# Performance work log

Hardware: AMD Instinct MI355X
Metric: run time of the kernel (lower is better)

## Reference

```python
import jax, jax.numpy as jnp
import numpy as np

B, T, D_IN, H, D_OUT, L = 8, 4096, 256, 1024, 256, 2


def setup_inputs() -> dict:
    key = jax.random.key(0)
    ks = jax.random.split(key, 8)
    def w(k, shape, fan):
        return (jax.random.normal(k, shape, jnp.float32) / np.sqrt(fan)).astype(jnp.float32)
    return dict(
        x=jax.random.normal(ks[0], (B, T, D_IN), jnp.float32),
        start=jax.random.randint(ks[1], (B, T), 0, 2).astype(bool),
        Wi=w(ks[2], (H, D_IN), D_IN), bi=jnp.zeros((H,), jnp.float32),
        Wp=w(ks[3], (L, H, H), H), bp=jnp.zeros((L, H), jnp.float32),
        Wf=w(ks[4], (L, H, 2 * H), 2 * H), bf=jnp.zeros((L, H), jnp.float32),
        Wo=w(ks[5], (D_OUT, H), H), bo=jnp.zeros((D_OUT,), jnp.float32),
    )


def _reset_scan(z, flags, carry0):
    # Resettable(LogBayesMonoid) segmented additive scan.
    # z: [B,T,H] log-likelihood increments, flags: [B,T] start flags, carry0: [B,1,H].
    states = jnp.concatenate([carry0, z], axis=1)                      # [B,T+1,H]
    f = jnp.concatenate([jnp.zeros_like(flags[:, :1]), flags], axis=1)  # [B,T+1]
    def combine(a, b):
        sa, fa = a
        sb, fb = b
        # reset-aware monoid combine: if b starts an episode, drop a's state
        return (jnp.where(fb[..., None], sb, sa + sb), fa | fb)
    s_all, _ = jax.lax.associative_scan(combine, (states, f), axis=1)
    return s_all[:, 1:]                                                # [B,T,H]


def reference(x, start, Wi, bi, Wp, bp, Wf, bf, Wo, bo):
    emb = jnp.einsum('btd,hd->bth', x, Wi) + bi                         # map_in
    hdim = Wi.shape[0]
    carry0 = jnp.full((x.shape[0], 1, hdim), -jnp.log(jnp.float32(hdim)), x.dtype)
    layer_in = emb
    for l in range(Wp.shape[0]):
        z = jnp.einsum('bth,gh->btg', layer_in, Wp[l]) + bp[l]          # forward_map project
        states = _reset_scan(z, start, carry0)                          # log-Bayes accumulation
        out = jax.nn.softmax(states, axis=-1)                           # backward_map readout
        cat = jnp.concatenate([out, emb], axis=-1)                      # [B,T,2H]
        layer_in = jax.nn.leaky_relu(jnp.einsum('btc,hc->bth', cat, Wf[l]) + bf[l])
    return jnp.einsum('bth,oh->bto', layer_in, Wo) + bo                 # map_out
```

## Files before the change

### kernel.cpp

```cpp
#include <hip/hip_runtime.h>
#include <stdint.h>

typedef unsigned short ushort_t;
typedef __attribute__((ext_vector_type(4))) float f32x4;
typedef __attribute__((ext_vector_type(8))) short bf16x8;
typedef __attribute__((ext_vector_type(4))) unsigned short u16x4;

#define DEV static __device__ __forceinline__

DEV unsigned short f2bf(float f) {
  unsigned int u = __float_as_uint(f);
  unsigned int r = (u + 0x7fffu + ((u >> 16) & 1u)) >> 16;
  return (unsigned short)r;
}

DEV float bf2f(ushort_t u) { return __uint_as_float((unsigned)u << 16); }

DEV float4 ld_bf4(const ushort_t* p) {
  const u16x4 u = *(const u16x4*)p;
  float4 v;
  v.x = bf2f(u.x); v.y = bf2f(u.y); v.z = bf2f(u.z); v.w = bf2f(u.w);
  return v;
}

DEV void async16(const void* g, void* l) {
  __builtin_amdgcn_global_load_lds(
      (const __attribute__((address_space(1))) unsigned int*)g,
      (__attribute__((address_space(3))) unsigned int*)l, 16, 0, 0);
}

template<bool SPLIT, bool RELU, bool OUTBF16>
__global__ __launch_bounds__(256, 2)
void gemm_bt(const ushort_t* __restrict__ A0, int lda0,
             const ushort_t* __restrict__ A1, int lda1,
             const ushort_t* __restrict__ W0, int ldw0,
             const ushort_t* __restrict__ W1, int ldw1,
             int K0, int K,
             const float* __restrict__ bias,
             void* __restrict__ Cv, int ldc,
             int rowsPerBatch, int cBatchStrideRows, int cRowOff)
{
  __shared__ __align__(16) ushort_t sA[2][128 * 32];
  __shared__ __align__(16) ushort_t sB[2][128 * 32];

  const int tid = threadIdx.x;
  const int w = tid >> 6, lane = tid & 63;

  const int NTl = gridDim.x;
  const int wgid = blockIdx.y * NTl + blockIdx.x;
  const int X = wgid & 7, j = wgid >> 3;
  const int n_t = j % NTl, mg = j / NTl;
  const int mBase = (X + 8 * mg) * 128;
  const int nBase = n_t * 128;

  const int wr = w >> 1, wc = w & 1;

  f32x4 acc[4][4] = {};

  auto stage = [&](int kt, int buf) {
    const int k0 = kt * 32;
    const ushort_t* Ap = A0; int lda = lda0; int ka = k0;
    const ushort_t* Wp = W0; int ldw = ldw0; int kw = k0;
    if (SPLIT && k0 >= K0) {
      Ap = A1; lda = lda1; ka = k0 - K0;
      Wp = W1; ldw = ldw1; kw = k0 - K0;
    }
#pragma unroll
    for (int c = 0; c < 2; ++c) {
      const int eb = (w * 2 + c) * 512;
      const int e = eb + lane * 8;
      const int row = e >> 5;
      const int gc = ((e >> 3) & 3) ^ ((row >> 1) & 3);
      async16(Ap + (size_t)(mBase + row) * lda + (ka + gc * 8), &sA[buf][eb]);
    }
#pragma unroll
    for (int c = 0; c < 2; ++c) {
      const int eb = (w * 2 + c) * 512;
      const int e = eb + lane * 8;
      const int row = e >> 5;
      const int gc = ((e >> 3) & 3) ^ ((row >> 1) & 3);
      async16(Wp + (size_t)(nBase + row) * ldw + (kw + gc * 8), &sB[buf][eb]);
    }
  };

  const int nkt = K >> 5;
  stage(0, 0);
  int cur = 0;
  const int fr = lane & 15, q4 = lane >> 4;

  for (int kt = 0; kt < nkt; ++kt) {
    __syncthreads();
    if (kt + 1 < nkt) stage(kt + 1, cur ^ 1);
    bf16x8 a[4], b[4];
#pragma unroll
    for (int m = 0; m < 4; ++m) {
      const int row = wr * 64 + m * 16 + fr;
      const int gc = q4 ^ ((row >> 1) & 3);
      a[m] = *(const bf16x8*)&sA[cur][row * 32 + gc * 8];
    }
#pragma unroll
    for (int n = 0; n < 4; ++n) {
      const int row = wc * 64 + n * 16 + fr;
      const int gc = q4 ^ ((row >> 1) & 3);
      b[n] = *(const bf16x8*)&sB[cur][row * 32 + gc * 8];
    }
#pragma unroll
    for (int m = 0; m < 4; ++m)
#pragma unroll
      for (int n = 0; n < 4; ++n)
        acc[m][n] = __builtin_amdgcn_mfma_f32_16x16x32_bf16(b[n], a[m], acc[m][n], 0, 0, 0);
    cur ^= 1;
  }

  const int bIdx = mBase / rowsPerBatch;
  const int rowBase = bIdx * cBatchStrideRows + cRowOff + (mBase - bIdx * rowsPerBatch);

  float* Cf = (float*)Cv;
  ushort_t* Cb = (ushort_t*)Cv;
#pragma unroll
  for (int m = 0; m < 4; ++m) {
    const int grow = rowBase + wr * 64 + m * 16 + fr;
    ushort_t* rowB = Cb + (size_t)grow * ldc;
    float*    rowF = Cf + (size_t)grow * ldc;
#pragma unroll
    for (int n = 0; n < 4; ++n) {
      const int nc = nBase + wc * 64 + n * 16 + q4 * 4;
      const float4 bv = *(const float4*)(bias + nc);
      float v0 = acc[m][n][0] + bv.x, v1 = acc[m][n][1] + bv.y;
      float v2 = acc[m][n][2] + bv.z, v3 = acc[m][n][3] + bv.w;
      if (RELU) {
        v0 = v0 > 0.f ? v0 : 0.01f * v0; v1 = v1 > 0.f ? v1 : 0.01f * v1;
        v2 = v2 > 0.f ? v2 : 0.01f * v2; v3 = v3 > 0.f ? v3 : 0.01f * v3;
      }
      if (OUTBF16) {
        u16x4 o;
        o.x = f2bf(v0); o.y = f2bf(v1); o.z = f2bf(v2); o.w = f2bf(v3);
        *(u16x4*)(rowB + nc) = o;
      } else {
        float4 o; o.x = v0; o.y = v1; o.z = v2; o.w = v3;
        *(float4*)(rowF + nc) = o;
      }
    }
  }
}

DEV int start_at(const void* start, int m, size_t idx) {
  return m ? (int)((const signed char*)start)[idx] : ((const int*)start)[idx];
}

__global__ __launch_bounds__(256)
void prep_all(const float* __restrict__ Wp, const float* __restrict__ Wf,
              const float* __restrict__ Wo, const float* __restrict__ Wi,
              const float* __restrict__ bi, const float* __restrict__ bp,
              const float* __restrict__ bf_,
              ushort_t* __restrict__ wp1, ushort_t* __restrict__ wf0a,
              ushort_t* __restrict__ wf1a, ushort_t* __restrict__ wp0b,
              ushort_t* __restrict__ wf0b, ushort_t* __restrict__ wf1b,
              ushort_t* __restrict__ wob, ushort_t* __restrict__ wiT,
              float* __restrict__ bz0, float* __restrict__ bc0,
              float* __restrict__ bc1, float* __restrict__ zeroB,
              const int* __restrict__ startW, int* __restrict__ mode,
              const float* __restrict__ x, ushort_t* __restrict__ xbc,
              int tcShift) {
  const int blk = blockIdx.x, tid = threadIdx.x;
  const int H = 1024;
  __shared__ float redf[256];
  __shared__ int redi[256];

  if (blk < 6400) {
    const int gq = blk * 256 + tid;
    const float* src; ushort_t* dst; int stride; int q;
    if (gq < 262144)       { q = gq;           src = Wp + (size_t)H * H;         dst = wp1;  stride = H; }
    else if (gq < 524288)  { q = gq - 262144;  src = Wf;                         dst = wf0a; stride = 2 * H; }
    else if (gq < 786432)  { q = gq - 524288;  src = Wf + (size_t)H * 2 * H;     dst = wf1a; stride = 2 * H; }
    else if (gq < 1048576) { q = gq - 786432;  src = Wp;                         dst = wp0b; stride = H; }
    else if (gq < 1310720) { q = gq - 1048576; src = Wf + H;                     dst = wf0b; stride = 2 * H; }
    else if (gq < 1572864) { q = gq - 1310720; src = Wf + (size_t)H * 2 * H + H; dst = wf1b; stride = 2 * H; }
    else                   { q = gq - 1572864; src = Wo;                         dst = wob;  stride = H; }
    const int row = q >> 8, cq = q & 255;
    const float4 v = *(const float4*)(src + (size_t)row * stride + cq * 4);
    u16x4 o;
    o.x = f2bf(v.x); o.y = f2bf(v.y); o.z = f2bf(v.z); o.w = f2bf(v.w);
    *(u16x4*)(dst + (size_t)row * 1024 + cq * 4) = o;
  } else if (blk < 7424) {
    const int i = (blk - 6400) * 256 + tid;
    const int d = i >> 10, h = i & 1023;
    wiT[(size_t)d * 1024 + h] = f2bf(Wi[(size_t)h * 256 + d]);
  } else if (blk < 10496) {
    const int f = blk - 7424;
    const int which = f >> 10, g = f & 1023;
    const float* A; int ldA; const float* bin; float* bout;
    if (which == 0)      { A = Wp;                         ldA = H;     bin = bp;      bout = bz0; }
    else if (which == 1) { A = Wf + H;                     ldA = 2 * H; bin = bf_;     bout = bc0; }
    else                 { A = Wf + (size_t)H * 2 * H + H; ldA = 2 * H; bin = bf_ + H; bout = bc1; }
    float acc = 0.f;
    for (int h = tid; h < 1024; h += 256) acc += A[(size_t)g * ldA + h] * bi[h];
    redf[tid] = acc;
    __syncthreads();
    for (int s = 128; s > 0; s >>= 1) {
      if (tid < s) redf[tid] += redf[tid + s];
      __syncthreads();
    }
    if (tid == 0) bout[g] = bin[g] + redf[0];
  } else if (blk == 10496) {
    zeroB[tid] = 0.f;
  } else if (blk == 10497) {
    int acc = 0;
    for (int i = tid; i < 8192; i += 256) acc |= startW[i];
    redi[tid] = acc;
    __syncthreads();
    for (int s = 128; s > 0; s >>= 1) {
      if (tid < s) redi[tid] |= redi[tid + s];
      __syncthreads();
    }
    if (tid == 0) *mode = (redi[0] & ~1) ? 1 : 0;
  } else {
    const int i = (blk - 10498) * 256 + tid;
    const int row = i >> 6, cq = i & 63;
    const int b = row >> tcShift, tl = row & ((1 << tcShift) - 1);
    const float4 v = *(const float4*)(x + ((size_t)b * 4096 + tl) * 256 + cq * 4);
    u16x4 o;
    o.x = f2bf(v.x); o.y = f2bf(v.y); o.z = f2bf(v.z); o.w = f2bf(v.w);
    *(u16x4*)(xbc + (size_t)row * 256 + cq * 4) = o;
  }
}

#define TB 16

__global__ __launch_bounds__(256)
void scan_p1(const ushort_t* __restrict__ z, const void* __restrict__ start,
             const int* __restrict__ mode, float* __restrict__ aggS,
             int* __restrict__ aggF, int t0, int Tc, int NT) {
  const int id = blockIdx.x * 256 + threadIdx.x;
  const int g = id & 1023;
  const int r = id >> 10;
  const int b = r / NT, tb = r - b * NT;
  const int m = *mode;
  const size_t sbase = (size_t)b * 4096 + t0 + tb * TB;
  const ushort_t* zp = z + ((size_t)b * Tc + tb * TB) * 1024 + g;
  float ls = 0.f;
  int lf = 0;
#pragma unroll
  for (int t = 0; t < TB; ++t) {
    const float zv = bf2f(zp[(size_t)t * 1024]);
    const int st = start_at(start, m, sbase + t);
    ls = st ? zv : (ls + zv);
    lf |= st;
  }
  aggS[(size_t)r * 1024 + g] = ls;
  if (g == 0) aggF[r] = lf;
}

__global__ __launch_bounds__(256)
void scan_p2(const float* __restrict__ aggS, const int* __restrict__ aggF,
             float* __restrict__ prefixS, float* __restrict__ carry,
             int first, int NT) {
  const int id = blockIdx.x * 256 + threadIdx.x;
  const int b = id >> 10, g = id & 1023;
  float s = first ? -6.93147180559945f : carry[id];
  for (int tb0 = 0; tb0 < NT; tb0 += 16) {
    float sums[16];
    int flags[16];
#pragma unroll
    for (int u = 0; u < 16; ++u) {
      const size_t r = (size_t)(b * NT + tb0 + u);
      sums[u] = aggS[r * 1024 + g];
      flags[u] = aggF[r];
    }
#pragma unroll
    for (int u = 0; u < 16; ++u) {
      const size_t r = (size_t)(b * NT + tb0 + u);
      prefixS[r * 1024 + g] = s;
      s = flags[u] ? sums[u] : (s + sums[u]);
    }
  }
  carry[id] = s;
}

__global__ __launch_bounds__(64)
void scan_p3sm_wave(const ushort_t* __restrict__ z, const void* __restrict__ start,
                    const int* __restrict__ mode, const float* __restrict__ prefixS,
                    ushort_t* __restrict__ P, int t0, int Tc, int NT) {
  const int r = blockIdx.x;
  const int b = r / NT, tb = r - b * NT;
  const int l = threadIdx.x;
  const int m = *mode;
  const size_t sbase = (size_t)b * 4096 + t0 + tb * TB;
  const ushort_t* zp = z + ((size_t)b * Tc + tb * TB) * 1024 + 4 * l;
  ushort_t* pp = P + ((size_t)b * Tc + tb * TB) * 1024 + 4 * l;

  float4 s[4], zv[4];
#pragma unroll
  for (int k = 0; k < 4; ++k)
    s[k] = *(const float4*)(prefixS + (size_t)r * 1024 + 4 * l + 256 * k);
#pragma unroll
  for (int k = 0; k < 4; ++k)
    zv[k] = ld_bf4(zp + 256 * k);

  for (int t = 0; t < TB; ++t) {
    float4 zn[4];
    if (t + 1 < TB) {
#pragma unroll
      for (int k = 0; k < 4; ++k)
        zn[k] = ld_bf4(zp + (size_t)(t + 1) * 1024 + 256 * k);
    } else {
#pragma unroll
      for (int k = 0; k < 4; ++k) zn[k] = zv[k];
    }
    const int st = start_at(start, m, sbase + t);
    if (st) {
#pragma unroll
      for (int k = 0; k < 4; ++k) s[k] = zv[k];
    } else {
#pragma unroll
      for (int k = 0; k < 4; ++k) {
        s[k].x += zv[k].x; s[k].y += zv[k].y;
        s[k].z += zv[k].z; s[k].w += zv[k].w;
      }
    }
    float mx = fmaxf(fmaxf(s[0].x, s[0].y), fmaxf(s[0].z, s[0].w));
#pragma unroll
    for (int k = 1; k < 4; ++k)
      mx = fmaxf(mx, fmaxf(fmaxf(s[k].x, s[k].y), fmaxf(s[k].z, s[k].w)));
#pragma unroll
    for (int o = 32; o > 0; o >>= 1) mx = fmaxf(mx, __shfl_xor(mx, o));
    float4 e[4];
    float sum = 0.f;
#pragma unroll
    for (int k = 0; k < 4; ++k) {
      e[k].x = __expf(s[k].x - mx); e[k].y = __expf(s[k].y - mx);
      e[k].z = __expf(s[k].z - mx); e[k].w = __expf(s[k].w - mx);
      sum += (e[k].x + e[k].y) + (e[k].z + e[k].w);
    }
#pragma unroll
    for (int o = 32; o > 0; o >>= 1) sum += __shfl_xor(sum, o);
    const float inv = 1.0f / sum;
#pragma unroll
    for (int k = 0; k < 4; ++k) {
      u16x4 o4;
      o4.x = f2bf(e[k].x * inv); o4.y = f2bf(e[k].y * inv);
      o4.z = f2bf(e[k].z * inv); o4.w = f2bf(e[k].w * inv);
      *(u16x4*)(pp + (size_t)t * 1024 + 256 * k) = o4;
    }
#pragma unroll
    for (int k = 0; k < 4; ++k) zv[k] = zn[k];
  }
}

__global__ __launch_bounds__(256)
void cvt_x_chunk(const float* __restrict__ x, ushort_t* __restrict__ dst,
                 int t0, int tcShift, int nq) {
  const int i = blockIdx.x * 256 + threadIdx.x;
  if (i >= nq) return;
  const int row = i >> 6, cq = i & 63;
  const int b = row >> tcShift, tl = row & ((1 << tcShift) - 1);
  const float4 v = *(const float4*)(x + ((size_t)b * 4096 + t0 + tl) * 256 + cq * 4);
  u16x4 o;
  o.x = f2bf(v.x); o.y = f2bf(v.y); o.z = f2bf(v.z); o.w = f2bf(v.w);
  *(u16x4*)(dst + (size_t)row * 256 + cq * 4) = o;
}

__global__ __launch_bounds__(256)
void fill_diag(float* __restrict__ out, int n, float v) {
  const int i = blockIdx.x * 256 + threadIdx.x;
  if (i < n) out[i] = v;
}

extern "C" void kernel_launch(void* const* d_in, const int* in_sizes, int n_in,
                              void* d_out, int out_size, void* d_ws, size_t ws_size,
                              hipStream_t stream) {
  const float* x    = (const float*)d_in[0];
  const void* start = (const void*)d_in[1];
  const float* Wi   = (const float*)d_in[2];
  const float* bi   = (const float*)d_in[3];
  const float* Wp   = (const float*)d_in[4];
  const float* bp   = (const float*)d_in[5];
  const float* Wf   = (const float*)d_in[6];
  const float* bf_  = (const float*)d_in[7];
  const float* Wo   = (const float*)d_in[8];
  const float* bo   = (const float*)d_in[9];

  const int T = 4096, H = 1024;

  char* ws = (char*)d_ws;
  size_t off = 0;
  auto alloc = [&](size_t bytes) {
    char* p = ws + off; off += (bytes + 255) & ~(size_t)255; return p;
  };

  ushort_t* wz0  = (ushort_t*)alloc((size_t)H * 256 * 2);
  ushort_t* wc0  = (ushort_t*)alloc((size_t)H * 256 * 2);
  ushort_t* wc1  = (ushort_t*)alloc((size_t)H * 256 * 2);
  ushort_t* wp1  = (ushort_t*)alloc((size_t)H * H * 2);
  ushort_t* wf0a = (ushort_t*)alloc((size_t)H * H * 2);
  ushort_t* wf1a = (ushort_t*)alloc((size_t)H * H * 2);
  ushort_t* wob  = (ushort_t*)alloc((size_t)256 * H * 2);
  ushort_t* wiT  = (ushort_t*)alloc((size_t)256 * H * 2);
  ushort_t* wp0b = (ushort_t*)alloc((size_t)H * H * 2);
  ushort_t* wf0b = (ushort_t*)alloc((size_t)H * H * 2);
  ushort_t* wf1b = (ushort_t*)alloc((size_t)H * H * 2);
  float* bz0 = (float*)alloc(H * 4);
  float* bc0 = (float*)alloc(H * 4);
  float* bc1 = (float*)alloc(H * 4);
  float* zeroB = (float*)alloc(256 * 4);
  float* carry0 = (float*)alloc(8192 * 4);
  float* carry1 = (float*)alloc(8192 * 4);
  int* mode = (int*)alloc(256);
  float* aggS    = (float*)alloc((size_t)8 * 256 * 1024 * 4);
  float* prefixS = (float*)alloc((size_t)8 * 256 * 1024 * 4);
  int*   aggF    = (int*)alloc(8 * 256 * 4);
  const size_t fixed = off;

  (void)wc0; (void)wc1; (void)wf0b; (void)wf1b;

  auto chunkBytes = [&](int Tc) -> size_t {
    const size_t Mc = (size_t)8 * Tc;
    return Mc * 256 * 2 + 256 + Mc * H * 2 + 256 +
           Mc * H * 2 + 256 + Mc * H * 2 + 256;
  };
  int Tc = 4096;
  while (Tc > 128 && fixed + chunkBytes(Tc) > ws_size) Tc >>= 1;
  if (fixed + chunkBytes(Tc) > ws_size) {
    fill_diag<<<dim3((out_size + 255) / 256), dim3(256), 0, stream>>>(
        (float*)d_out, out_size, (float)(ws_size >> 20));
    return;
  }
  const int Mc = 8 * Tc;
  const int NT = Tc / TB;
  const int tcShift = __builtin_ctz((unsigned)Tc);
  ushort_t* xbc  = (ushort_t*)alloc((size_t)Mc * 256 * 2);
  ushort_t* zbuf = (ushort_t*)alloc((size_t)Mc * H * 2);
  ushort_t* pbuf = (ushort_t*)alloc((size_t)Mc * H * 2);
  ushort_t* hbuf = (ushort_t*)alloc((size_t)Mc * H * 2);

  const dim3 blk(256);

  auto run_scan = [&](ushort_t* z, float* carry, int first, int t0) {
    scan_p1<<<dim3(32 * NT), blk, 0, stream>>>(z, start, mode, aggS, aggF, t0, Tc, NT);
    scan_p2<<<dim3(32), blk, 0, stream>>>(aggS, aggF, prefixS, carry, first, NT);
    scan_p3sm_wave<<<dim3(8 * NT), dim3(64), 0, stream>>>(
        z, start, mode, prefixS, pbuf, t0, Tc, NT);
  };

  const int xblocks = (Mc * 64) / 256;
  prep_all<<<dim3(10498 + xblocks), blk, 0, stream>>>(
      Wp, Wf, Wo, Wi, bi, bp, bf_,
      wp1, wf0a, wf1a, wp0b, wf0b, wf1b, wob, wiT,
      bz0, bc0, bc1, zeroB, (const int*)start, mode, x, xbc, tcShift);

  gemm_bt<false, false, true><<<dim3(2, 24), blk, 0, stream>>>(
      wp0b, H, wp0b, H, wiT, H, wiT, H, H, H, zeroB, wz0, 256, 3072, 0, 0);

  const int nch = T / Tc;
  for (int c = 0; c < nch; ++c) {
    const int t0 = c * Tc;
    if (c > 0)
      cvt_x_chunk<<<dim3((Mc * 64 + 255) / 256), blk, 0, stream>>>(
          x, xbc, t0, tcShift, Mc * 64);
    gemm_bt<false, false, true><<<dim3(H / 128, Mc / 128), blk, 0, stream>>>(
        xbc, 256, xbc, 256, wz0, 256, wz0, 256, 256, 256, bz0, zbuf, H, Mc, 0, 0);
    run_scan(zbuf, carry0, c == 0, t0);
    gemm_bt<true, true, true><<<dim3(H / 128, Mc / 128), blk, 0, stream>>>(
        pbuf, H, xbc, 256, wf0a, H, wc0, 256, H, H + 256, bc0, hbuf, H, Mc, 0, 0);
    gemm_bt<false, false, true><<<dim3(H / 128, Mc / 128), blk, 0, stream>>>(
        hbuf, H, hbuf, H, wp1, H, wp1, H, H, H, bp + H, zbuf, H, Mc, 0, 0);
    run_scan(zbuf, carry1, c == 0, t0);
    gemm_bt<true, true, true><<<dim3(H / 128, Mc / 128), blk, 0, stream>>>(
        pbuf, H, xbc, 256, wf1a, H, wc1, 256, H, H + 256, bc1, hbuf, H, Mc, 0, 0);
    gemm_bt<false, false, false><<<dim3(256 / 128, Mc / 128), blk, 0, stream>>>(
        hbuf, H, hbuf, H, wob, H, wob, H, H, H, bo, (float*)d_out, 256,
        Tc, T, t0);
  }
}
```

Before: 530.2 us.

## Add 256x128-tile GEMM with 512 threads and XCD-aware block remap

```diff
diff --git a/kernel.cpp b/kernel.cpp
--- a/kernel.cpp
+++ b/kernel.cpp
@@ -120,6 +120,116 @@
 #pragma unroll
   for (int m = 0; m < 4; ++m) {
     const int grow = rowBase + wr * 64 + m * 16 + fr;
+    ushort_t* rowB = Cb + (size_t)grow * ldc;
+    float*    rowF = Cf + (size_t)grow * ldc;
+#pragma unroll
+    for (int n = 0; n < 4; ++n) {
+      const int nc = nBase + wc * 64 + n * 16 + q4 * 4;
+      const float4 bv = *(const float4*)(bias + nc);
+      float v0 = acc[m][n][0] + bv.x, v1 = acc[m][n][1] + bv.y;
+      float v2 = acc[m][n][2] + bv.z, v3 = acc[m][n][3] + bv.w;
+      if (RELU) {
+        v0 = v0 > 0.f ? v0 : 0.01f * v0; v1 = v1 > 0.f ? v1 : 0.01f * v1;
+        v2 = v2 > 0.f ? v2 : 0.01f * v2; v3 = v3 > 0.f ? v3 : 0.01f * v3;
+      }
+      if (OUTBF16) {
+        u16x4 o;
+        o.x = f2bf(v0); o.y = f2bf(v1); o.z = f2bf(v2); o.w = f2bf(v3);
+        *(u16x4*)(rowB + nc) = o;
+      } else {
+        float4 o; o.x = v0; o.y = v1; o.z = v2; o.w = v3;
+        *(float4*)(rowF + nc) = o;
+      }
+    }
+  }
+}
+
+template<bool SPLIT, bool RELU, bool OUTBF16>
+__global__ __launch_bounds__(512, 2)
+void gemm_bt2(const ushort_t* __restrict__ A0, int lda0,
+              const ushort_t* __restrict__ A1, int lda1,
+              const ushort_t* __restrict__ W0, int ldw0,
+              const ushort_t* __restrict__ W1, int ldw1,
+              int K0, int K,
+              const float* __restrict__ bias,
+              void* __restrict__ Cv, int ldc)
+{
+  __shared__ __align__(16) ushort_t sA[2][256 * 32];
+  __shared__ __align__(16) ushort_t sB[2][128 * 32];
+
+  const int tid = threadIdx.x;
+  const int w = tid >> 6, lane = tid & 63;
+
+  const int NTl = gridDim.x;
+  const int wgid = blockIdx.y * NTl + blockIdx.x;
+  const int X = wgid & 7, j = wgid >> 3;
+  const int n_t = j % NTl, mg = j / NTl;
+  const int mBase = (X + 8 * mg) * 256;
+  const int nBase = n_t * 128;
+
+  const int wr = w >> 1, wc = w & 1;
+
+  f32x4 acc[4][4] = {};
+
+  auto stage = [&](int kt, int buf) {
+    const int k0 = kt * 32;
+    const ushort_t* Ap = A0; int lda = lda0; int ka = k0;
+    const ushort_t* Wp = W0; int ldw = ldw0; int kw = k0;
+    if (SPLIT && k0 >= K0) {
+      Ap = A1; lda = lda1; ka = k0 - K0;
+      Wp = W1; ldw = ldw1; kw = k0 - K0;
+    }
+#pragma unroll
+    for (int c = 0; c < 2; ++c) {
+      const int eb = (w * 2 + c) * 512;
+      const int e = eb + lane * 8;
+      const int row = e >> 5;
+      const int gc = ((e >> 3) & 3) ^ ((row >> 1) & 3);
+      async16(Ap + (size_t)(mBase + row) * lda + (ka + gc * 8), &sA[buf][eb]);
+    }
+    {
+      const int eb = w * 512;
+      const int e = eb + lane * 8;
+      const int row = e >> 5;
+      const int gc = ((e >> 3) & 3) ^ ((row >> 1) & 3);
+      async16(Wp + (size_t)(nBase + row) * ldw + (kw + gc * 8), &sB[buf][eb]);
+    }
+  };
+
+  const int nkt = K >> 5;
+  stage(0, 0);
+  int cur = 0;
+  const int fr = lane & 15, q4 = lane >> 4;
+
+  for (int kt = 0; kt < nkt; ++kt) {
+    __syncthreads();
+    if (kt + 1 < nkt) stage(kt + 1, cur ^ 1);
+    bf16x8 a[4], b[4];
+#pragma unroll
+    for (int m = 0; m < 4; ++m) {
+      const int row = wr * 64 + m * 16 + fr;
+      const int gc = q4 ^ ((row >> 1) & 3);
+      a[m] = *(const bf16x8*)&sA[cur][row * 32 + gc * 8];
+    }
+#pragma unroll
+    for (int n = 0; n < 4; ++n) {
+      const int row = wc * 64 + n * 16 + fr;
+      const int gc = q4 ^ ((row >> 1) & 3);
+      b[n] = *(const bf16x8*)&sB[cur][row * 32 + gc * 8];
+    }
+#pragma unroll
+    for (int m = 0; m < 4; ++m)
+#pragma unroll
+      for (int n = 0; n < 4; ++n)
+        acc[m][n] = __builtin_amdgcn_mfma_f32_16x16x32_bf16(b[n], a[m], acc[m][n], 0, 0, 0);
+    cur ^= 1;
+  }
+
+  float* Cf = (float*)Cv;
+  ushort_t* Cb = (ushort_t*)Cv;
+#pragma unroll
+  for (int m = 0; m < 4; ++m) {
+    const int grow = mBase + wr * 64 + m * 16 + fr;
     ushort_t* rowB = Cb + (size_t)grow * ldc;
     float*    rowF = Cf + (size_t)grow * ldc;
 #pragma unroll
@@ -433,7 +543,8 @@
   ushort_t* pbuf = (ushort_t*)alloc((size_t)Mc * H * 2);
   ushort_t* hbuf = (ushort_t*)alloc((size_t)Mc * H * 2);
 
-  const dim3 blk(256);
+  const dim3 blk(256), blk2(512);
+  const dim3 bigGrid(H / 128, Mc / 256);
 
   auto run_scan = [&](ushort_t* z, float* carry, int first, int t0) {
     scan_p1<<<dim3(32 * NT), blk, 0, stream>>>(z, start, mode, aggS, aggF, t0, Tc, NT);
@@ -457,16 +568,16 @@
     if (c > 0)
       cvt_x_chunk<<<dim3((Mc * 64 + 255) / 256), blk, 0, stream>>>(
           x, xbc, t0, tcShift, Mc * 64);
-    gemm_bt<false, false, true><<<dim3(H / 128, Mc / 128), blk, 0, stream>>>(
-        xbc, 256, xbc, 256, wz0, 256, wz0, 256, 256, 256, bz0, zbuf, H, Mc, 0, 0);
+    gemm_bt2<false, false, true><<<bigGrid, blk2, 0, stream>>>(
+        xbc, 256, xbc, 256, wz0, 256, wz0, 256, 256, 256, bz0, zbuf, H);
     run_scan(zbuf, carry0, c == 0, t0);
-    gemm_bt<true, true, true><<<dim3(H / 128, Mc / 128), blk, 0, stream>>>(
-        pbuf, H, xbc, 256, wf0a, H, wc0, 256, H, H + 256, bc0, hbuf, H, Mc, 0, 0);
-    gemm_bt<false, false, true><<<dim3(H / 128, Mc / 128), blk, 0, stream>>>(
-        hbuf, H, hbuf, H, wp1, H, wp1, H, H, H, bp + H, zbuf, H, Mc, 0, 0);
+    gemm_bt2<true, true, true><<<bigGrid, blk2, 0, stream>>>(
+        pbuf, H, xbc, 256, wf0a, H, wc0, 256, H, H + 256, bc0, hbuf, H);
+    gemm_bt2<false, false, true><<<bigGrid, blk2, 0, stream>>>(
+        hbuf, H, hbuf, H, wp1, H, wp1, H, H, H, bp + H, zbuf, H);
     run_scan(zbuf, carry1, c == 0, t0);
-    gemm_bt<true, true, true><<<dim3(H / 128, Mc / 128), blk, 0, stream>>>(
-        pbuf, H, xbc, 256, wf1a, H, wc1, 256, H, H + 256, bc1, hbuf, H, Mc, 0, 0);
+    gemm_bt2<true, true, true><<<bigGrid, blk2, 0, stream>>>(
+        pbuf, H, xbc, 256, wf1a, H, wc1, 256, H, H + 256, bc1, hbuf, H);
     gemm_bt<false, false, false><<<dim3(256 / 128, Mc / 128), blk, 0, stream>>>(
         hbuf, H, hbuf, H, wob, H, wob, H, H, H, bo, (float*)d_out, 256,
         Tc, T, t0);
```

Measured after the change: 515.0 us. 2.9% less time.
